# Optimization experiments

Measured on AMD Instinct MI355X. Metric: run time of the kernel, lower is better.

The kernel has to match this reference:

```python
import jax, jax.numpy as jnp
from jax import lax
import numpy as np

INPUT_SIZE, HIDDEN, NUM_LAYERS, NUM_CLASSES = 128, 256, 2, 100
B, T = 256, 512


def _lstm_layer(x, W_ih, W_hh, b_ih, b_hh):
    # x: [B, T, in]; W_ih: [4H, in]; W_hh: [4H, H]; gate order i,f,g,o (PyTorch)
    Bsz = x.shape[0]
    H = W_hh.shape[1]
    x_proj = jnp.einsum('bti,gi->btg', x, W_ih) + b_ih + b_hh  # [B, T, 4H]
    h0 = jnp.zeros((Bsz, H), x.dtype)
    c0 = jnp.zeros((Bsz, H), x.dtype)

    def step(carry, xt):
        h, c = carry
        gates = xt + h @ W_hh.T  # [B, 4H]
        i, f, g, o = jnp.split(gates, 4, axis=-1)
        i = jax.nn.sigmoid(i)
        f = jax.nn.sigmoid(f)
        g = jnp.tanh(g)
        o = jax.nn.sigmoid(o)
        c = f * c + i * g
        h = o * jnp.tanh(c)
        return (h, c), h

    _, hs = lax.scan(step, (h0, c0), jnp.swapaxes(x_proj, 0, 1))  # hs: [T, B, H]
    return jnp.swapaxes(hs, 0, 1)  # [B, T, H]


def setup_inputs() -> dict:
    key = jax.random.key(0)
    ks = jax.random.split(key, 12)
    s_in = 1.0 / np.sqrt(HIDDEN)
    inp = {
        'x': jax.random.normal(ks[0], (B, T, INPUT_SIZE), jnp.float32),
        'W_ih0': jax.random.uniform(ks[1], (4 * HIDDEN, INPUT_SIZE), jnp.float32, -s_in, s_in),
        'W_hh0': jax.random.uniform(ks[2], (4 * HIDDEN, HIDDEN), jnp.float32, -s_in, s_in),
        'b_ih0': jax.random.uniform(ks[3], (4 * HIDDEN,), jnp.float32, -s_in, s_in),
        'b_hh0': jax.random.uniform(ks[4], (4 * HIDDEN,), jnp.float32, -s_in, s_in),
        'W_ih1': jax.random.uniform(ks[5], (4 * HIDDEN, HIDDEN), jnp.float32, -s_in, s_in),
        'W_hh1': jax.random.uniform(ks[6], (4 * HIDDEN, HIDDEN), jnp.float32, -s_in, s_in),
        'b_ih1': jax.random.uniform(ks[7], (4 * HIDDEN,), jnp.float32, -s_in, s_in),
        'b_hh1': jax.random.uniform(ks[8], (4 * HIDDEN,), jnp.float32, -s_in, s_in),
        'fc_w': jax.random.uniform(ks[9], (NUM_CLASSES, HIDDEN), jnp.float32, -s_in, s_in),
        'fc_b': jax.random.uniform(ks[10], (NUM_CLASSES,), jnp.float32, -s_in, s_in),
    }
    return inp


def reference(x, W_ih0, W_hh0, b_ih0, b_hh0, W_ih1, W_hh1, b_ih1, b_hh1, fc_w, fc_b):
    h = _lstm_layer(x, W_ih0, W_hh0, b_ih0, b_hh0)
    h = _lstm_layer(h, W_ih1, W_hh1, b_ih1, b_hh1)
    return h[:, -1, :] @ fc_w.T + fc_b  # [B, num_classes]
```

## Files before the change

kernel.cpp:

```cpp
#include <hip/hip_runtime.h>
#include <math.h>

namespace {

constexpr int kB  = 256;
constexpr int kT  = 512;
constexpr int kIn = 128;
constexpr int kH  = 256;
constexpr int kG  = 1024;
constexpr int kNC = 100;
constexpr int kCT = 64;
constexpr int kNCh = kT / kCT;

typedef __bf16 bf16x8 __attribute__((ext_vector_type(8)));
typedef float f32x4 __attribute__((ext_vector_type(4)));
typedef int i32x4 __attribute__((ext_vector_type(4)));
typedef unsigned short u16;
static_assert(sizeof(bf16x8) == 16, "bf16x8 must be 4 VGPRs");

__device__ __forceinline__ float sigm(float x) {
  return __builtin_amdgcn_rcpf(1.0f + __expf(-x));
}
__device__ __forceinline__ float tanh_f(float x) {
  const float e = __expf(-2.0f * x);
  return (1.0f - e) * __builtin_amdgcn_rcpf(1.0f + e);
}
__device__ __forceinline__ u16 f2bf(float f) {
  return __builtin_bit_cast(u16, (__bf16)f);
}
__device__ __forceinline__ float bf2f(u16 v) {
  return __builtin_bit_cast(float, ((unsigned)v) << 16);
}

__device__ __forceinline__ void glds16(const void* g, void* l) {
  __builtin_amdgcn_global_load_lds(
      (const __attribute__((address_space(1))) void*)g,
      (__attribute__((address_space(3))) void*)l, 16, 0, 0);
}
__device__ __forceinline__ void glds16_llc(const void* g, void* l) {
  __builtin_amdgcn_global_load_lds(
      (const __attribute__((address_space(1))) void*)g,
      (__attribute__((address_space(3))) void*)l, 16, 0, 17);
}
__device__ __forceinline__ void st_bf16_llc(u16* p, u16 v) {
  asm volatile("global_store_short %0, %1, off sc0 sc1"
               :: "v"((unsigned long long)(uintptr_t)p), "v"(v) : "memory");
}
__device__ __forceinline__ void st_i32_llc(int* p, int v) {
  asm volatile("global_store_dword %0, %1, off sc0 sc1"
               :: "v"((unsigned long long)(uintptr_t)p), "v"(v) : "memory");
}
__device__ __forceinline__ int poll16_min(const int* p) {
  i32x4 a, b, c, d;
  asm volatile(
      "global_load_dwordx4 %0, %4, off sc0 sc1\n\t"
      "global_load_dwordx4 %1, %5, off sc0 sc1\n\t"
      "global_load_dwordx4 %2, %6, off sc0 sc1\n\t"
      "global_load_dwordx4 %3, %7, off sc0 sc1\n\t"
      "s_waitcnt vmcnt(0)"
      : "=v"(a), "=v"(b), "=v"(c), "=v"(d)
      : "v"((unsigned long long)(uintptr_t)p),
        "v"((unsigned long long)(uintptr_t)(p + 4)),
        "v"((unsigned long long)(uintptr_t)(p + 8)),
        "v"((unsigned long long)(uintptr_t)(p + 12))
      : "memory");
  int m = a.x;
  m = min(m, a.y); m = min(m, a.z); m = min(m, a.w);
  m = min(m, b.x); m = min(m, b.y); m = min(m, b.z); m = min(m, b.w);
  m = min(m, c.x); m = min(m, c.y); m = min(m, c.z); m = min(m, c.w);
  m = min(m, d.x); m = min(m, d.y); m = min(m, d.z); m = min(m, d.w);
  return m;
}

__global__ __launch_bounds__(256) void pack_whh_frag(
    const float* __restrict__ whh, u16* __restrict__ wpk) {
  const int idx = blockIdx.x * 256 + threadIdx.x;
  const int e  = idx & 7;
  const int l  = (idx >> 3) & 63;
  const int kb = (idx >> 9) & 7;
  const int g  = (idx >> 12) & 3;
  const int wv = idx >> 14;
  const int n = (g << 8) | (wv << 4) | (l & 15);
  const int k = (kb << 5) | (((l >> 4) & 3) << 3) | e;
  wpk[idx] = f2bf(whh[n * kH + k]);
}

template <int K>
__global__ __launch_bounds__(256) void pack_wih_frag(
    const float* __restrict__ w, u16* __restrict__ wp) {
  constexpr int kbBits = (K == 128) ? 2 : 3;
  const int idx = blockIdx.x * 256 + threadIdx.x;
  const int e  = idx & 7;
  const int l  = (idx >> 3) & 63;
  const int kb = (idx >> 9) & ((K / 32) - 1);
  const int n16 = idx >> (9 + kbBits);
  const int n = (n16 << 4) | (l & 15);
  const int k = (kb << 5) | (((l >> 4) & 3) << 3) | e;
  wp[idx] = f2bf(w[n * K + k]);
}

__global__ __launch_bounds__(256) void conv_x(
    const float* __restrict__ x, u16* __restrict__ xbf) {
  const int f4 = blockIdx.x * 256 + threadIdx.x;
  const int rowid = f4 >> 5;
  const int c4 = f4 & 31;
  const int b = rowid >> 9, t = rowid & 511;
  const float4 v = reinterpret_cast<const float4*>(x)[f4];
  ushort4 o;
  o.x = f2bf(v.x); o.y = f2bf(v.y); o.z = f2bf(v.z); o.w = f2bf(v.w);
  reinterpret_cast<ushort4*>(xbf)[(t * 256 + b) * 32 + c4] = o;
}

template <int K>
__global__ __launch_bounds__(256, 4) void gemm_mfma(
    const u16* __restrict__ A, const u16* __restrict__ Bp,
    const float* __restrict__ b1, const float* __restrict__ b2,
    u16* __restrict__ P2) {
  constexpr int NKB = K / 32;
  const int g = blockIdx.x, mt = blockIdx.y;
  const int tt = mt >> 2, bq = mt & 3;
  const int tid = threadIdx.x, w = tid >> 6, l = tid & 63;

  __shared__ __align__(16) unsigned char smem[40960];
  u16* albuf = (u16*)smem;
  u16* bbuf  = (u16*)(smem + 8192);
  u16* sout  = (u16*)smem;

  const u16* Ab = A + ((size_t)(tt * 256 + bq * 64 + w * 16 + (l & 15))) * K +
                  ((l >> 4) & 3) * 8;
  const u16* Bb = Bp + ((size_t)((g * 16 + w * 4) * NKB) * 64 + l) * 8;

  float bb[4];
#pragma unroll
  for (int j = 0; j < 4; ++j) {
    const int n = g * 256 + (w * 4 + j) * 16 + (l & 15);
    bb[j] = b1[n] + b2[n];
  }

  f32x4 acc[4][4];
#pragma unroll
  for (int mf = 0; mf < 4; ++mf)
#pragma unroll
    for (int nf = 0; nf < 4; ++nf) acc[mf][nf] = f32x4{0.f, 0.f, 0.f, 0.f};

#define STAGE(kb, buf)                                                     \
  {                                                                        \
    glds16(Ab + (kb) * 32, albuf + ((buf) * 4 + w) * 512);                 \
    _Pragma("unroll") for (int j = 0; j < 4; ++j)                          \
        glds16(Bb + ((size_t)(j * NKB + (kb)) * 64) * 8,                   \
               bbuf + ((buf) * 16 + w * 4 + j) * 512);                     \
  }

  STAGE(0, 0);
#pragma unroll
  for (int kb = 0; kb < NKB; ++kb) {
    __syncthreads();
    if (kb + 1 < NKB) STAGE(kb + 1, (kb + 1) & 1);
    const int buf = kb & 1;
    bf16x8 af[4], bf[4];
#pragma unroll
    for (int mf = 0; mf < 4; ++mf)
      af[mf] = *reinterpret_cast<const bf16x8*>(albuf + (buf * 4 + mf) * 512 + l * 8);
#pragma unroll
    for (int nf = 0; nf < 4; ++nf)
      bf[nf] = *reinterpret_cast<const bf16x8*>(bbuf + (buf * 16 + w * 4 + nf) * 512 + l * 8);
#pragma unroll
    for (int mf = 0; mf < 4; ++mf)
#pragma unroll
      for (int nf = 0; nf < 4; ++nf)
        acc[mf][nf] = __builtin_amdgcn_mfma_f32_16x16x32_bf16(
            af[mf], bf[nf], acc[mf][nf], 0, 0, 0);
  }
#undef STAGE

  __syncthreads();
#pragma unroll
  for (int mf = 0; mf < 4; ++mf)
#pragma unroll
    for (int nf = 0; nf < 4; ++nf) {
      ushort4 p;
      p.x = f2bf(acc[mf][nf][0] + bb[nf]);
      p.y = f2bf(acc[mf][nf][1] + bb[nf]);
      p.z = f2bf(acc[mf][nf][2] + bb[nf]);
      p.w = f2bf(acc[mf][nf][3] + bb[nf]);
      *reinterpret_cast<ushort4*>(
          sout + (mf * 16 + w * 4 + nf) * 256 + (l & 15) * 16 + ((l >> 4) & 3) * 4) = p;
    }
  __syncthreads();
#pragma unroll
  for (int i = 0; i < 8; ++i) {
    const int chunk = i * 8 + (tid >> 5);
    const int mf = chunk >> 4, wc = chunk & 15;
    const size_t dst =
        ((((size_t)(bq * 4 + mf) * 64 + tt) * 16 + wc) * 4 + g) * 256 +
        (tid & 31) * 8;
    *reinterpret_cast<uint4*>(P2 + dst) =
        *reinterpret_cast<const uint4*>(sout + (mf * 16 + wc) * 256 + (tid & 31) * 8);
  }
}

__global__ __launch_bounds__(256, 1) void lstm_rec_dual(
    const u16* __restrict__ P2_0, const u16* __restrict__ wpk_0,
    float* __restrict__ cs_0, u16* __restrict__ Ho_0, float* __restrict__ hl_0,
    u16* __restrict__ hx_0, int* __restrict__ tg_0, int first_0,
    const u16* __restrict__ P2_1, const u16* __restrict__ wpk_1,
    float* __restrict__ cs_1, u16* __restrict__ Ho_1, float* __restrict__ hl_1,
    u16* __restrict__ hx_1, int* __restrict__ tg_1, int first_1) {
  const int role = blockIdx.x >> 6;
  const u16* P2  = role ? P2_1 : P2_0;
  if (!P2) return;
  const u16* wpk = role ? wpk_1 : wpk_0;
  float* cstate  = role ? cs_1 : cs_0;
  u16* HoutBf    = role ? Ho_1 : Ho_0;
  float* hlast   = role ? hl_1 : hl_0;
  u16* hx        = role ? hx_1 : hx_0;
  int* tags      = role ? tg_1 : tg_0;
  const int first = role ? first_1 : first_0;

  const int bid6 = blockIdx.x & 63;
  const int tid = threadIdx.x;
  const int ug = tid >> 6;
  const int l  = tid & 63;
  const int bblk = bid6 & 15;
  const int hs   = bid6 >> 4;
  const int R0 = bblk << 4;
  const int wv16 = (hs << 2) | ug;
  const int jj = (wv16 << 4) | (l & 15);
  const int mg = ((l >> 4) & 3) << 2;
  const int rowb = R0 + mg;

  __shared__ __align__(16) u16 albuf[2][8][512];

  int* tgb = tags + bblk * 1024;
  u16* hx0 = hx;
  u16* hx1 = hx + (size_t)kB * kH;

  bf16x8 wr[4][8];
#pragma unroll
  for (int g = 0; g < 4; ++g)
#pragma unroll
    for (int kb = 0; kb < 8; ++kb) {
      wr[g][kb] = *reinterpret_cast<const bf16x8*>(
          wpk + (size_t)(((wv16 * 4 + g) * 8 + kb) * 64 + l) * 8);
      asm volatile("" : "+v"(wr[g][kb]));
    }

  f32x4 c4;
  float hnew[4];
  if (first) {
#pragma unroll
    for (int r = 0; r < 4; ++r) c4[r] = 0.f;
  } else {
#pragma unroll
    for (int r = 0; r < 4; ++r) c4[r] = cstate[(rowb + r) * kH + jj];
  }

  const u16* __restrict__ Pb =
      P2 + ((size_t)bblk * 64 * 16 + wv16) * 1024 + ((l & 15) << 4) + mg;
  ushort4 pf[4];
#pragma unroll
  for (int g = 0; g < 4; ++g)
    pf[g] = *reinterpret_cast<const ushort4*>(Pb + (g << 8));

  const int gkb = ug << 1;
#define ISSUE_GLDS(buf, bsel)                                               \
  {                                                                         \
    _Pragma("unroll") for (int q = 0; q < 2; ++q) {                         \
      const int kb = gkb + q;                                               \
      glds16_llc((buf) + ((size_t)(R0 + (l & 15))) * 256 + kb * 32 +        \
                     ((l >> 4) & 3) * 8,                                    \
                 &albuf[bsel][kb][0]);                                      \
    }                                                                       \
  }

  ISSUE_GLDS(hx0, 0);

  for (int tt = 0; tt < kCT; ++tt) {
    __syncthreads();

    f32x4 acc[4];
#pragma unroll
    for (int g = 0; g < 4; ++g) {
      acc[g][0] = bf2f(pf[g].x);
      acc[g][1] = bf2f(pf[g].y);
      acc[g][2] = bf2f(pf[g].z);
      acc[g][3] = bf2f(pf[g].w);
    }
    if (tt + 1 < kCT) {
#pragma unroll
      for (int g = 0; g < 4; ++g)
        pf[g] = *reinterpret_cast<const ushort4*>(
            Pb + (size_t)(tt + 1) * 16384 + (g << 8));
    }

    const u16* ab = &albuf[tt & 1][0][0];
#pragma unroll
    for (int kb = 0; kb < 8; ++kb) {
      const bf16x8 a = *reinterpret_cast<const bf16x8*>(ab + kb * 512 + l * 8);
      acc[0] = __builtin_amdgcn_mfma_f32_16x16x32_bf16(a, wr[0][kb], acc[0], 0, 0, 0);
      acc[1] = __builtin_amdgcn_mfma_f32_16x16x32_bf16(a, wr[1][kb], acc[1], 0, 0, 0);
      acc[2] = __builtin_amdgcn_mfma_f32_16x16x32_bf16(a, wr[2][kb], acc[2], 0, 0, 0);
      acc[3] = __builtin_amdgcn_mfma_f32_16x16x32_bf16(a, wr[3][kb], acc[3], 0, 0, 0);
    }

#pragma unroll
    for (int r = 0; r < 4; ++r) {
      const float ig = sigm(acc[0][r]);
      const float fg = sigm(acc[1][r]);
      const float gg = tanh_f(acc[2][r]);
      const float og = sigm(acc[3][r]);
      const float cc = fg * c4[r] + ig * gg;
      c4[r] = cc;
      hnew[r] = og * tanh_f(cc);
    }

    u16* hw = ((tt + 1) & 1) ? hx1 : hx0;
#pragma unroll
    for (int r = 0; r < 4; ++r)
      st_bf16_llc(hw + ((size_t)(rowb + r) << 8) + jj, f2bf(hnew[r]));

    if (tt + 1 < kCT) {
      const int want = tt + 1;
      asm volatile("s_waitcnt vmcnt(0)" ::: "memory");
      if (l == 0) st_i32_llc(tgb + want * 16 + (hs * 4 + ug), want);
      if (HoutBf) {
#pragma unroll
        for (int r = 0; r < 4; ++r)
          HoutBf[((size_t)tt * 256 + rowb + r) * 256 + jj] = f2bf(hnew[r]);
      }
      while (poll16_min(tgb + want * 16) < want)
        __builtin_amdgcn_s_sleep(1);
      const u16* hr = ((tt + 1) & 1) ? hx1 : hx0;
      ISSUE_GLDS(hr, (tt + 1) & 1);
    } else {
      if (HoutBf) {
#pragma unroll
        for (int r = 0; r < 4; ++r)
          HoutBf[((size_t)tt * 256 + rowb + r) * 256 + jj] = f2bf(hnew[r]);
      }
      if (hlast) {
#pragma unroll
        for (int r = 0; r < 4; ++r)
          hlast[(rowb + r) * kH + jj] = hnew[r];
      }
    }
  }
#undef ISSUE_GLDS

#pragma unroll
  for (int r = 0; r < 4; ++r) cstate[(rowb + r) * kH + jj] = c4[r];
}

__global__ __launch_bounds__(128) void fc_kernel(
    const float* __restrict__ hlast, const float* __restrict__ fcw,
    const float* __restrict__ fcb, float* __restrict__ out) {
  const int b = blockIdx.x;
  const int n = threadIdx.x;
  __shared__ float sh[kH];
  sh[n] = hlast[b * kH + n];
  sh[n + 128] = hlast[b * kH + n + 128];
  __syncthreads();
  if (n < kNC) {
    float a = fcb[n];
    const float* wrow = fcw + n * kH;
#pragma unroll 8
    for (int k = 0; k < kH; ++k) a += sh[k] * wrow[k];
    out[b * kNC + n] = a;
  }
}

}

extern "C" void kernel_launch(void* const* d_in, const int* in_sizes, int n_in,
                              void* d_out, int out_size, void* d_ws, size_t ws_size,
                              hipStream_t stream) {
  (void)in_sizes; (void)n_in; (void)out_size; (void)ws_size;
  const float* x    = (const float*)d_in[0];
  const float* Wih0 = (const float*)d_in[1];
  const float* Whh0 = (const float*)d_in[2];
  const float* bih0 = (const float*)d_in[3];
  const float* bhh0 = (const float*)d_in[4];
  const float* Wih1 = (const float*)d_in[5];
  const float* Whh1 = (const float*)d_in[6];
  const float* bih1 = (const float*)d_in[7];
  const float* bhh1 = (const float*)d_in[8];
  const float* fcw  = (const float*)d_in[9];
  const float* fcb  = (const float*)d_in[10];
  float* out = (float*)d_out;

  char* base = (char*)d_ws;
  size_t off = 0;
  auto take = [&](size_t sz) { char* p = base + off; off += (sz + 255) & ~(size_t)255; return p; };
  const size_t szP2   = (size_t)kB * kCT * kG * 2;
  const size_t szXbf  = (size_t)kT * kB * kIn * 2;
  const size_t szH0   = (size_t)kCT * kB * kH * 2;
  const size_t szC    = (size_t)kB * kH * 4;
  const size_t szHx   = (size_t)2 * kB * kH * 2;
  const size_t szWih0 = (size_t)64 * (kIn / 32) * 512 * 2;
  const size_t szWih1 = (size_t)64 * (kH / 32) * 512 * 2;
  const size_t szWhh  = (size_t)262144 * 2;
  const size_t szTags = (size_t)16 * 16 * 1024 * 4;

  u16* P2a  = (u16*)take(szP2);
  u16* P2b  = (u16*)take(szP2);
  u16* xbf  = (u16*)take(szXbf);
  u16* H0bf = (u16*)take(szH0);
  float* c0s = (float*)take(szC);
  float* c1s = (float*)take(szC);
  float* h1s = (float*)take(szC);
  u16* hxA = (u16*)take(szHx);
  u16* hxB = (u16*)take(szHx);
  u16* WpIh0 = (u16*)take(szWih0);
  u16* WpIh1 = (u16*)take(szWih1);
  u16* Wpk0 = (u16*)take(szWhh);
  u16* Wpk1 = (u16*)take(szWhh);
  int* tags = (int*)take(szTags);

  hipMemsetAsync(tags, 0, szTags, stream);
  hipMemsetAsync(hxA, 0, szHx, stream);
  hipMemsetAsync(hxB, 0, szHx, stream);

  conv_x<<<dim3(16384), dim3(256), 0, stream>>>(x, xbf);
  pack_wih_frag<kIn><<<dim3(512), dim3(256), 0, stream>>>(Wih0, WpIh0);
  pack_wih_frag<kH><<<dim3(1024), dim3(256), 0, stream>>>(Wih1, WpIh1);
  pack_whh_frag<<<dim3(1024), dim3(256), 0, stream>>>(Whh0, Wpk0);
  pack_whh_frag<<<dim3(1024), dim3(256), 0, stream>>>(Whh1, Wpk1);

  auto tslot = [&](int s) { return tags + (size_t)s * 16 * 1024; };

  gemm_mfma<kIn><<<dim3(4, 256), dim3(256), 0, stream>>>(
      xbf, WpIh0, bih0, bhh0, P2a);
  lstm_rec_dual<<<dim3(128), dim3(256), 0, stream>>>(
      P2a, Wpk0, c0s, H0bf, nullptr, hxA, tslot(0), 1,
      nullptr, nullptr, nullptr, nullptr, nullptr, nullptr, nullptr, 0);
  for (int ch = 1; ch < kNCh; ++ch) {
    gemm_mfma<kH><<<dim3(4, 256), dim3(256), 0, stream>>>(
        H0bf, WpIh1, bih1, bhh1, P2b);
    gemm_mfma<kIn><<<dim3(4, 256), dim3(256), 0, stream>>>(
        xbf + (size_t)ch * kCT * kB * kIn, WpIh0, bih0, bhh0, P2a);
    lstm_rec_dual<<<dim3(128), dim3(256), 0, stream>>>(
        P2a, Wpk0, c0s, H0bf, nullptr, hxA, tslot(2 * ch), (ch == 0) ? 1 : 0,
        P2b, Wpk1, c1s, nullptr, h1s, hxB, tslot(2 * (ch - 1) + 1),
        (ch == 1) ? 1 : 0);
  }
  gemm_mfma<kH><<<dim3(4, 256), dim3(256), 0, stream>>>(
      H0bf, WpIh1, bih1, bhh1, P2b);
  lstm_rec_dual<<<dim3(128), dim3(256), 0, stream>>>(
      nullptr, nullptr, nullptr, nullptr, nullptr, nullptr, nullptr, 0,
      P2b, Wpk1, c1s, nullptr, h1s, hxB, tslot(2 * (kNCh - 1) + 1), 0);
  fc_kernel<<<dim3(kB), dim3(128), 0, stream>>>(h1s, fcw, fcb, out);
}
```

Measured before the change: 1.859 ms.

## Overlap next chunk's layer-0 input GEMM with recurrent kernel via extra blocks

The layer-0 input projection for the next time chunk now runs as extra blocks (indices 128 and up) inside the recurrent kernel launch, and the projection buffer is double-buffered so it can be written while the current chunk is read. The goal is to hide the GEMM behind the latency-bound recurrence, which uses only 128 blocks, and to drop one launch per chunk. The risk is that the GEMM blocks compete for CUs, cache and memory bandwidth with the persistent spin-waiting recurrent blocks. If the recurrent blocks are not all resident at once, the cross-block polling could also be delayed. The poll asm outputs are also made early-clobber so the output registers cannot overlap the address inputs.

Measured after the change: 1.817 ms (median of 2 runs). -2.3%, faster.

```diff
diff --git a/kernel.cpp b/kernel.cpp
--- a/kernel.cpp
+++ b/kernel.cpp
@@ -58,7 +58,7 @@
       "global_load_dwordx4 %2, %6, off sc0 sc1\n\t"
       "global_load_dwordx4 %3, %7, off sc0 sc1\n\t"
       "s_waitcnt vmcnt(0)"
-      : "=v"(a), "=v"(b), "=v"(c), "=v"(d)
+      : "=&v"(a), "=&v"(b), "=&v"(c), "=&v"(d)
       : "v"((unsigned long long)(uintptr_t)p),
         "v"((unsigned long long)(uintptr_t)(p + 4)),
         "v"((unsigned long long)(uintptr_t)(p + 8)),
@@ -112,16 +112,15 @@
 }
 
 template <int K>
-__global__ __launch_bounds__(256, 4) void gemm_mfma(
+__device__ __forceinline__ void gemm_body(
     const u16* __restrict__ A, const u16* __restrict__ Bp,
     const float* __restrict__ b1, const float* __restrict__ b2,
-    u16* __restrict__ P2) {
+    u16* __restrict__ P2, int gbid, unsigned char* smem) {
   constexpr int NKB = K / 32;
-  const int g = blockIdx.x, mt = blockIdx.y;
+  const int g = gbid & 3, mt = gbid >> 2;
   const int tt = mt >> 2, bq = mt & 3;
   const int tid = threadIdx.x, w = tid >> 6, l = tid & 63;
 
-  __shared__ __align__(16) unsigned char smem[40960];
   u16* albuf = (u16*)smem;
   u16* bbuf  = (u16*)(smem + 8192);
   u16* sout  = (u16*)smem;
@@ -199,13 +198,32 @@
   }
 }
 
-__global__ __launch_bounds__(256, 1) void lstm_rec_dual(
+template <int K>
+__global__ __launch_bounds__(256, 4) void gemm_flat(
+    const u16* __restrict__ A, const u16* __restrict__ Bp,
+    const float* __restrict__ b1, const float* __restrict__ b2,
+    u16* __restrict__ P2) {
+  __shared__ __align__(16) unsigned char smem[40960];
+  gemm_body<K>(A, Bp, b1, b2, P2, blockIdx.x, smem);
+}
+
+__global__ __launch_bounds__(256, 1) void fused_step(
     const u16* __restrict__ P2_0, const u16* __restrict__ wpk_0,
     float* __restrict__ cs_0, u16* __restrict__ Ho_0, float* __restrict__ hl_0,
     u16* __restrict__ hx_0, int* __restrict__ tg_0, int first_0,
     const u16* __restrict__ P2_1, const u16* __restrict__ wpk_1,
     float* __restrict__ cs_1, u16* __restrict__ Ho_1, float* __restrict__ hl_1,
-    u16* __restrict__ hx_1, int* __restrict__ tg_1, int first_1) {
+    u16* __restrict__ hx_1, int* __restrict__ tg_1, int first_1,
+    const u16* __restrict__ Ag, const u16* __restrict__ Bg,
+    const float* __restrict__ b1g, const float* __restrict__ b2g,
+    u16* __restrict__ Pg) {
+  __shared__ __align__(16) unsigned char smem[40960];
+
+  if (blockIdx.x >= 128) {
+    if (Ag) gemm_body<kIn>(Ag, Bg, b1g, b2g, Pg, blockIdx.x - 128, smem);
+    return;
+  }
+
   const int role = blockIdx.x >> 6;
   const u16* P2  = role ? P2_1 : P2_0;
   if (!P2) return;
@@ -229,7 +247,7 @@
   const int mg = ((l >> 4) & 3) << 2;
   const int rowb = R0 + mg;
 
-  __shared__ __align__(16) u16 albuf[2][8][512];
+  u16 (*albuf)[8][512] = reinterpret_cast<u16 (*)[8][512]>(smem);
 
   int* tgb = tags + bblk * 1024;
   u16* hx0 = hx;
@@ -401,7 +419,8 @@
   const size_t szWhh  = (size_t)262144 * 2;
   const size_t szTags = (size_t)16 * 16 * 1024 * 4;
 
-  u16* P2a  = (u16*)take(szP2);
+  u16* P2a0 = (u16*)take(szP2);
+  u16* P2a1 = (u16*)take(szP2);
   u16* P2b  = (u16*)take(szP2);
   u16* xbf  = (u16*)take(szXbf);
   u16* H0bf = (u16*)take(szH0);
@@ -427,26 +446,36 @@
   pack_whh_frag<<<dim3(1024), dim3(256), 0, stream>>>(Whh1, Wpk1);
 
   auto tslot = [&](int s) { return tags + (size_t)s * 16 * 1024; };
-
-  gemm_mfma<kIn><<<dim3(4, 256), dim3(256), 0, stream>>>(
-      xbf, WpIh0, bih0, bhh0, P2a);
-  lstm_rec_dual<<<dim3(128), dim3(256), 0, stream>>>(
-      P2a, Wpk0, c0s, H0bf, nullptr, hxA, tslot(0), 1,
-      nullptr, nullptr, nullptr, nullptr, nullptr, nullptr, nullptr, 0);
+  auto p2a = [&](int ch) { return (ch & 1) ? P2a1 : P2a0; };
+  const size_t ckElems = (size_t)kCT * kB * kIn;
+
+  gemm_flat<kIn><<<dim3(1024), dim3(256), 0, stream>>>(
+      xbf, WpIh0, bih0, bhh0, P2a0);
+
+  fused_step<<<dim3(1152), dim3(256), 0, stream>>>(
+      P2a0, Wpk0, c0s, H0bf, nullptr, hxA, tslot(0), 1,
+      nullptr, nullptr, nullptr, nullptr, nullptr, nullptr, nullptr, 0,
+      xbf + ckElems, WpIh0, bih0, bhh0, P2a1);
+
   for (int ch = 1; ch < kNCh; ++ch) {
-    gemm_mfma<kH><<<dim3(4, 256), dim3(256), 0, stream>>>(
+    gemm_flat<kH><<<dim3(1024), dim3(256), 0, stream>>>(
         H0bf, WpIh1, bih1, bhh1, P2b);
-    gemm_mfma<kIn><<<dim3(4, 256), dim3(256), 0, stream>>>(
-        xbf + (size_t)ch * kCT * kB * kIn, WpIh0, bih0, bhh0, P2a);
-    lstm_rec_dual<<<dim3(128), dim3(256), 0, stream>>>(
-        P2a, Wpk0, c0s, H0bf, nullptr, hxA, tslot(2 * ch), (ch == 0) ? 1 : 0,
+    const bool haveG = (ch + 1 < kNCh);
+    const u16* gA = haveG ? xbf + (size_t)(ch + 1) * ckElems : nullptr;
+    u16* gP = haveG ? p2a(ch + 1) : nullptr;
+    const int grid = haveG ? 1152 : 128;
+    fused_step<<<dim3(grid), dim3(256), 0, stream>>>(
+        p2a(ch), Wpk0, c0s, H0bf, nullptr, hxA, tslot(2 * ch), 0,
         P2b, Wpk1, c1s, nullptr, h1s, hxB, tslot(2 * (ch - 1) + 1),
-        (ch == 1) ? 1 : 0);
-  }
-  gemm_mfma<kH><<<dim3(4, 256), dim3(256), 0, stream>>>(
+        (ch == 1) ? 1 : 0,
+        gA, WpIh0, bih0, bhh0, gP);
+  }
+
+  gemm_flat<kH><<<dim3(1024), dim3(256), 0, stream>>>(
       H0bf, WpIh1, bih1, bhh1, P2b);
-  lstm_rec_dual<<<dim3(128), dim3(256), 0, stream>>>(
+  fused_step<<<dim3(128), dim3(256), 0, stream>>>(
       nullptr, nullptr, nullptr, nullptr, nullptr, nullptr, nullptr, 0,
-      P2b, Wpk1, c1s, nullptr, h1s, hxB, tslot(2 * (kNCh - 1) + 1), 0);
+      P2b, Wpk1, c1s, nullptr, h1s, hxB, tslot(2 * (kNCh - 1) + 1), 0,
+      nullptr, nullptr, nullptr, nullptr, nullptr);
   fc_kernel<<<dim3(kB), dim3(128), 0, stream>>>(h1s, fcw, fcb, out);
 }
```
